# Kernel optimization log

Hardware: AMD Instinct MI355X
Metric: run time of the kernel (lower is better)

The kernel has to match this reference:

```python
import jax, jax.numpy as jnp
import numpy as np

N = 50000      # nodes
E = 800000     # edges (before self-loops)
DIN = 256      # in_channel
H = 1          # heads (PyG GATConv default)
C = 128        # out_channel per head
NEG_SLOPE = 0.2


def setup_inputs() -> dict:
    key = jax.random.key(0)
    k1, k2, k3, k4, k5 = jax.random.split(key, 5)
    x = jax.random.normal(k1, (N, DIN), jnp.float32)
    # random edges guaranteed to have no self-loops (PyG removes then re-adds them)
    src = jax.random.randint(k2, (E,), 0, N, dtype=jnp.int32)
    off = jax.random.randint(k3, (E,), 1, N, dtype=jnp.int32)
    dst = (src + off) % N
    edge_index = jnp.stack([src, dst])  # [2, E], row0=source j, row1=target i
    W = jax.random.normal(k4, (DIN, H * C), jnp.float32) / np.sqrt(DIN)
    att = jax.random.normal(k5, (1, H, 2 * C), jnp.float32) * 0.1
    bias = jnp.zeros((H * C,), jnp.float32)
    return {"x": x, "edge_index": edge_index, "W": W, "att": att, "bias": bias}


def reference(x, edge_index, W, att, bias):
    n = x.shape[0]
    h = (x @ W).reshape(n, H, C)                       # [N,H,C]
    # add self-loops (PyG GATConv forward)
    loops = jnp.arange(n, dtype=edge_index.dtype)
    src = jnp.concatenate([edge_index[0], loops])       # [Et]
    dst = jnp.concatenate([edge_index[1], loops])       # [Et]
    h_i = h[dst]                                        # [Et,H,C] target feats
    h_j = h[src]                                        # [Et,H,C] source feats
    # per-edge attention logit: sum(cat(x_i, x_j) * att)
    alpha = jnp.sum(jnp.concatenate([h_i, h_j], axis=-1) * att, axis=-1)  # [Et,H]
    alpha = jax.nn.leaky_relu(alpha, NEG_SLOPE)
    # segment softmax grouped by destination node (numerically stable)
    amax = jax.ops.segment_max(alpha, dst, num_segments=n)  # [N,H]
    ex = jnp.exp(alpha - amax[dst])
    denom = jax.ops.segment_sum(ex, dst, num_segments=n)    # [N,H]
    a = ex / (denom[dst] + 1e-16)                            # [Et,H]
    # scatter-aggregate weighted source features to targets
    out = jax.ops.segment_sum(h_j * a[..., None], dst, num_segments=n)  # [N,H,C]
    return out.reshape(n, H * C) + bias
```

## Files before the change

kernel.cpp:

```cpp
#include <hip/hip_runtime.h>
#include <hip/hip_bf16.h>

constexpr int N_NODES = 50000;
constexpr int DIN     = 256;
constexpr int C_OUT   = 128;
constexpr int E_EDGES = 800000;
constexpr int ET      = E_EDGES + N_NODES;
constexpr float NEG_SLOPE = 0.2f;

constexpr int NHI      = 196;
constexpr int CAP      = 6144;
constexpr int PEPC     = 8192;
constexpr int NPB_PART = (ET + PEPC - 1) / PEPC;
constexpr int WCONV_BLOCKS = (DIN * C_OUT) / 256;
constexpr int GEMM_RPB    = 64;
constexpr int GEMM_BLOCKS = (N_NODES + GEMM_RPB - 1) / GEMM_RPB;
constexpr int AGG_NPB     = 32;
constexpr int AGG_BLOCKS  = (N_NODES + AGG_NPB - 1) / AGG_NPB;

typedef __attribute__((ext_vector_type(8))) short short8v;
typedef __attribute__((ext_vector_type(4))) float f32x4;

static __device__ __forceinline__ ushort f2bf(float f) {
    __hip_bfloat16 b = __float2bfloat16(f);
    return *reinterpret_cast<ushort*>(&b);
}
static __device__ __forceinline__ short f2bfs(float f) {
    __hip_bfloat16 b = __float2bfloat16(f);
    return *reinterpret_cast<short*>(&b);
}

__global__ __launch_bounds__(256) void part_wconv(const float* __restrict__ W,
                                                  const int* __restrict__ ei,
                                                  ushort* __restrict__ wt,
                                                  int* __restrict__ gcur,
                                                  int* __restrict__ ebuf) {
    const int t = threadIdx.x;
    if (blockIdx.x < NPB_PART) {
        __shared__ int hist[256], basel[256], curl[256];
        const int c = blockIdx.x;
        hist[t] = 0;
        __syncthreads();
        #pragma unroll 4
        for (int i = 0; i < 32; i++) {
            const int e = c * PEPC + i * 256 + t;
            if (e < ET) {
                const int d = (e < E_EDGES) ? ei[E_EDGES + e] : (e - E_EDGES);
                atomicAdd(&hist[d >> 8], 1);
            }
        }
        __syncthreads();
        if (t < NHI) basel[t] = atomicAdd(&gcur[t], hist[t]);
        curl[t] = 0;
        __syncthreads();
        #pragma unroll 4
        for (int i = 0; i < 32; i++) {
            const int e = c * PEPC + i * 256 + t;
            if (e < ET) {
                int s, d;
                if (e < E_EDGES) { s = ei[e]; d = ei[E_EDGES + e]; }
                else             { s = e - E_EDGES; d = s; }
                const int hi = d >> 8;
                const int r = atomicAdd(&curl[hi], 1);
                const int pos = basel[hi] + r;
                if (pos < CAP) ebuf[(size_t)hi * CAP + pos] = ((d & 255) << 16) | s;
            }
        }
        return;
    }
    const int idx = (blockIdx.x - NPB_PART) * 256 + t;
    if (idx < DIN * C_OUT) {
        const int k = idx >> 7, col = idx & 127;
        const int ks = k >> 5, kgrp = (k >> 3) & 3, j = k & 7;
        const int cc = col >> 4, col16 = col & 15;
        wt[((ks * 8 + cc) * 64 + kgrp * 16 + col16) * 8 + j] = f2bf(W[idx]);
    }
}

__global__ __launch_bounds__(256) void gemm_mfma(const float* __restrict__ x,
                                                 const ushort* __restrict__ wt,
                                                 const float* __restrict__ att,
                                                 ushort* __restrict__ hb,
                                                 float* __restrict__ s_dst,
                                                 float* __restrict__ s_src) {
    __shared__ ushort lw[DIN * C_OUT / 2];
    const int t = threadIdx.x;
    const int lane = t & 63, wv = t >> 6;
    const int col16 = lane & 15, kgrp = lane >> 4;
    const int rowbase = blockIdx.x * GEMM_RPB + wv * 16;
    const int hrow = rowbase + col16;
    int r0 = hrow; if (r0 >= N_NODES) r0 = N_NODES - 1;
    const float* xr0 = x + (size_t)r0 * DIN + kgrp * 8;

    f32x4 acc[8] = {};
    const short8v* lwf = (const short8v*)lw;
    #pragma unroll
    for (int ph = 0; ph < 2; ph++) {
        if (ph) __syncthreads();
        {
            const uint4* src = (const uint4*)(wt + ph * (DIN * C_OUT / 2));
            uint4* dst = (uint4*)lw;
            #pragma unroll
            for (int i = 0; i < 8; i++) dst[t + i * 256] = src[t + i * 256];
        }
        short8v A0[4];
        #pragma unroll
        for (int ks = 0; ks < 4; ks++) {
            const int kg = ph * 4 + ks;
            const float4 v0 = *(const float4*)(xr0 + kg * 32);
            const float4 v1 = *(const float4*)(xr0 + kg * 32 + 4);
            short8v a;
            a[0] = f2bfs(v0.x); a[1] = f2bfs(v0.y); a[2] = f2bfs(v0.z); a[3] = f2bfs(v0.w);
            a[4] = f2bfs(v1.x); a[5] = f2bfs(v1.y); a[6] = f2bfs(v1.z); a[7] = f2bfs(v1.w);
            A0[ks] = a;
        }
        __syncthreads();
        #pragma unroll
        for (int ks = 0; ks < 4; ks++) {
            #pragma unroll
            for (int c = 0; c < 8; c++) {
                const short8v bfr = lwf[(ks * 8 + c) * 64 + lane];
                acc[c] = __builtin_amdgcn_mfma_f32_16x16x32_bf16(bfr, A0[ks], acc[c], 0, 0, 0);
            }
        }
    }

    const bool ok = (hrow < N_NODES);
    float pd = 0.f, ps = 0.f;
    #pragma unroll
    for (int c = 0; c < 8; c++) {
        const int colb = c * 16 + kgrp * 4;
        const float4 ad = *(const float4*)(att + colb);
        const float4 as = *(const float4*)(att + C_OUT + colb);
        pd += acc[c][0] * ad.x + acc[c][1] * ad.y + acc[c][2] * ad.z + acc[c][3] * ad.w;
        ps += acc[c][0] * as.x + acc[c][1] * as.y + acc[c][2] * as.z + acc[c][3] * as.w;
        if (ok) {
            uint2 pk;
            pk.x = (uint)(ushort)f2bf(acc[c][0]) | ((uint)(ushort)f2bf(acc[c][1]) << 16);
            pk.y = (uint)(ushort)f2bf(acc[c][2]) | ((uint)(ushort)f2bf(acc[c][3]) << 16);
            *(uint2*)(hb + (size_t)hrow * C_OUT + colb) = pk;
        }
    }
    pd += __shfl_xor(pd, 16); pd += __shfl_xor(pd, 32);
    ps += __shfl_xor(ps, 16); ps += __shfl_xor(ps, 32);
    if (kgrp == 0 && ok) { s_dst[hrow] = pd; s_src[hrow] = ps; }
}

__global__ __launch_bounds__(256) void final_kernel(const int* __restrict__ gcur,
                                                    const int* __restrict__ ebuf,
                                                    int2* __restrict__ offs2,
                                                    int* __restrict__ esrc) {
    __shared__ int histl[256], sA[256], sE[256], curl[256];
    const int t = threadIdx.x, hi = blockIdx.x;
    const int n = min(gcur[hi], CAP);
    const size_t segbase = (size_t)hi * CAP;
    histl[t] = 0;
    __syncthreads();
    for (int k = t; k < n; k += 256)
        atomicAdd(&histl[(ebuf[segbase + k] >> 16) & 255], 1);
    __syncthreads();
    const int v = histl[t];
    sA[t] = v;
    __syncthreads();
    #pragma unroll
    for (int off = 1; off < 256; off <<= 1) {
        const int y = (t >= off) ? sA[t - off] : 0;
        __syncthreads();
        sA[t] += y;
        __syncthreads();
    }
    sE[t] = sA[t] - v;
    curl[t] = 0;
    const int node = hi * 256 + t;
    if (node < N_NODES) {
        const int beg = (int)segbase + sE[t];
        offs2[node] = make_int2(beg, beg + v);
    }
    __syncthreads();
    for (int k = t; k < n; k += 256) {
        const int e2 = ebuf[segbase + k];
        const int lo = (e2 >> 16) & 255;
        const int r = atomicAdd(&curl[lo], 1);
        esrc[segbase + sE[lo] + r] = e2 & 0xFFFF;
    }
}

__global__ __launch_bounds__(256) void aggregate_kernel(
    const ushort* __restrict__ hb, const int2* __restrict__ offs2,
    const int* __restrict__ esrc, const float* __restrict__ s_dst,
    const float* __restrict__ s_src, const float* __restrict__ bias,
    float* __restrict__ out) {
    const int t = threadIdx.x;
    const int wv = t >> 6, lane = t & 63;
    const int sub = lane >> 3, l8 = lane & 7;
    const int node = blockIdx.x * AGG_NPB + wv * 8 + sub;
    const bool valid = (node < N_NODES);

    const int2 be = valid ? offs2[node] : make_int2(0, 0);
    const float sd = valid ? s_dst[node] : 0.f;
    float den = 0.f;
    float acc[16] = {};
    const uint4* __restrict__ h4 = (const uint4*)hb;

    for (int e = be.x; e < be.y; e++) {
        const int s = esrc[e];
        float a = sd + s_src[s];
        a = (a > 0.f) ? a : NEG_SLOPE * a;
        const float w = __expf(a);
        den += w;
        const uint4 hv0 = h4[(size_t)s * 16 + l8];
        const uint4 hv1 = h4[(size_t)s * 16 + 8 + l8];
        acc[0]  += w * __uint_as_float(hv0.x << 16);
        acc[1]  += w * __uint_as_float(hv0.x & 0xffff0000u);
        acc[2]  += w * __uint_as_float(hv0.y << 16);
        acc[3]  += w * __uint_as_float(hv0.y & 0xffff0000u);
        acc[4]  += w * __uint_as_float(hv0.z << 16);
        acc[5]  += w * __uint_as_float(hv0.z & 0xffff0000u);
        acc[6]  += w * __uint_as_float(hv0.w << 16);
        acc[7]  += w * __uint_as_float(hv0.w & 0xffff0000u);
        acc[8]  += w * __uint_as_float(hv1.x << 16);
        acc[9]  += w * __uint_as_float(hv1.x & 0xffff0000u);
        acc[10] += w * __uint_as_float(hv1.y << 16);
        acc[11] += w * __uint_as_float(hv1.y & 0xffff0000u);
        acc[12] += w * __uint_as_float(hv1.z << 16);
        acc[13] += w * __uint_as_float(hv1.z & 0xffff0000u);
        acc[14] += w * __uint_as_float(hv1.w << 16);
        acc[15] += w * __uint_as_float(hv1.w & 0xffff0000u);
    }
    if (!valid) return;
    const float inv = 1.f / (den + 1e-16f);
    float* op = out + (size_t)node * C_OUT;
    #pragma unroll
    for (int half = 0; half < 2; half++) {
        const int base = half * 64 + l8 * 8;
        const float4 b0 = *(const float4*)(bias + base);
        const float4 b1 = *(const float4*)(bias + base + 4);
        float4 o0 = make_float4(acc[half * 8 + 0] * inv + b0.x, acc[half * 8 + 1] * inv + b0.y,
                                acc[half * 8 + 2] * inv + b0.z, acc[half * 8 + 3] * inv + b0.w);
        float4 o1 = make_float4(acc[half * 8 + 4] * inv + b1.x, acc[half * 8 + 5] * inv + b1.y,
                                acc[half * 8 + 6] * inv + b1.z, acc[half * 8 + 7] * inv + b1.w);
        *(float4*)(op + base)     = o0;
        *(float4*)(op + base + 4) = o1;
    }
}

extern "C" void kernel_launch(void* const* d_in, const int* in_sizes, int n_in,
                              void* d_out, int out_size, void* d_ws, size_t ws_size,
                              hipStream_t stream) {
    const float* x    = (const float*)d_in[0];
    const int*   ei   = (const int*)d_in[1];
    const float* W    = (const float*)d_in[2];
    const float* att  = (const float*)d_in[3];
    const float* bias = (const float*)d_in[4];
    float* out = (float*)d_out;

    ushort* wt    = (ushort*)d_ws;
    ushort* hbuf  = wt + DIN * C_OUT;
    int*    ebuf  = (int*)(hbuf + (size_t)N_NODES * C_OUT);
    int*    esrc  = ebuf + (size_t)NHI * CAP;
    float*  s_src = (float*)(esrc + (size_t)NHI * CAP);
    float*  s_dst = s_src + N_NODES;
    int2*   offs2 = (int2*)(s_dst + N_NODES);
    int*    gcur  = (int*)(offs2 + N_NODES);

    hipMemsetAsync(gcur, 0, NHI * sizeof(int), stream);
    part_wconv<<<NPB_PART + WCONV_BLOCKS, 256, 0, stream>>>(W, ei, wt, gcur, ebuf);
    gemm_mfma<<<GEMM_BLOCKS, 256, 0, stream>>>(x, wt, att, hbuf, s_dst, s_src);
    final_kernel<<<NHI, 256, 0, stream>>>(gcur, ebuf, offs2, esrc);
    aggregate_kernel<<<AGG_BLOCKS, 256, 0, stream>>>(
        hbuf, offs2, esrc, s_dst, s_src, bias, out);
}
```

Measured before the change: 101.4 us.

## Fuse CSR finalize into GEMM launch with per-chunk fixed-slot partitioning

Partitioning now writes each chunk's edges into fixed-size per-(bucket,chunk) slots, so one histogram pass, the global atomics and the memset go away. The CSR finalize step runs as extra blocks of the GEMM launch, so one kernel launch is removed and it overlaps with the matmul. Self-loops are no longer stored as edges; the aggregation kernel seeds its accumulators with each node's own term instead. Edges beyond the 96 per bucket-chunk slot cap would be dropped silently. Finalize blocks now scan a sparse, padded segment with per-slot count checks.

```diff
diff --git a/kernel.cpp b/kernel.cpp
--- a/kernel.cpp
+++ b/kernel.cpp
@@ -5,18 +5,19 @@
 constexpr int DIN     = 256;
 constexpr int C_OUT   = 128;
 constexpr int E_EDGES = 800000;
-constexpr int ET      = E_EDGES + N_NODES;
 constexpr float NEG_SLOPE = 0.2f;
 
-constexpr int NHI      = 196;
-constexpr int CAP      = 6144;
-constexpr int PEPC     = 8192;
-constexpr int NPB_PART = (ET + PEPC - 1) / PEPC;
+constexpr int NHI  = 196;
+constexpr int NCH  = 98;
+constexpr int EPC  = 8192;
+constexpr int CPC  = 96;
+constexpr int SEG  = NCH * CPC;
+constexpr int CAPB = 6144;
 constexpr int WCONV_BLOCKS = (DIN * C_OUT) / 256;
-constexpr int GEMM_RPB    = 64;
-constexpr int GEMM_BLOCKS = (N_NODES + GEMM_RPB - 1) / GEMM_RPB;
-constexpr int AGG_NPB     = 32;
-constexpr int AGG_BLOCKS  = (N_NODES + AGG_NPB - 1) / AGG_NPB;
+constexpr int GEMM_RPB     = 64;
+constexpr int GEMM_BLOCKS  = (N_NODES + GEMM_RPB - 1) / GEMM_RPB;
+constexpr int AGG_NPB      = 32;
+constexpr int AGG_BLOCKS   = (N_NODES + AGG_NPB - 1) / AGG_NPB;
 
 typedef __attribute__((ext_vector_type(8))) short short8v;
 typedef __attribute__((ext_vector_type(4))) float f32x4;
@@ -33,42 +34,31 @@
 __global__ __launch_bounds__(256) void part_wconv(const float* __restrict__ W,
                                                   const int* __restrict__ ei,
                                                   ushort* __restrict__ wt,
-                                                  int* __restrict__ gcur,
+                                                  int* __restrict__ cnt2,
                                                   int* __restrict__ ebuf) {
     const int t = threadIdx.x;
-    if (blockIdx.x < NPB_PART) {
-        __shared__ int hist[256], basel[256], curl[256];
+    if (blockIdx.x < NCH) {
+        __shared__ int curl[256];
         const int c = blockIdx.x;
-        hist[t] = 0;
+        curl[t] = 0;
         __syncthreads();
         #pragma unroll 4
         for (int i = 0; i < 32; i++) {
-            const int e = c * PEPC + i * 256 + t;
-            if (e < ET) {
-                const int d = (e < E_EDGES) ? ei[E_EDGES + e] : (e - E_EDGES);
-                atomicAdd(&hist[d >> 8], 1);
-            }
-        }
-        __syncthreads();
-        if (t < NHI) basel[t] = atomicAdd(&gcur[t], hist[t]);
-        curl[t] = 0;
-        __syncthreads();
-        #pragma unroll 4
-        for (int i = 0; i < 32; i++) {
-            const int e = c * PEPC + i * 256 + t;
-            if (e < ET) {
-                int s, d;
-                if (e < E_EDGES) { s = ei[e]; d = ei[E_EDGES + e]; }
-                else             { s = e - E_EDGES; d = s; }
+            const int e = c * EPC + i * 256 + t;
+            if (e < E_EDGES) {
+                const int s = ei[e];
+                const int d = ei[E_EDGES + e];
                 const int hi = d >> 8;
                 const int r = atomicAdd(&curl[hi], 1);
-                const int pos = basel[hi] + r;
-                if (pos < CAP) ebuf[(size_t)hi * CAP + pos] = ((d & 255) << 16) | s;
+                if (r < CPC)
+                    ebuf[(size_t)(hi * NCH + c) * CPC + r] = ((d & 255) << 16) | s;
             }
         }
+        __syncthreads();
+        if (t < NHI) cnt2[t * NCH + c] = min(curl[t], CPC);
         return;
     }
-    const int idx = (blockIdx.x - NPB_PART) * 256 + t;
+    const int idx = (blockIdx.x - NCH) * 256 + t;
     if (idx < DIN * C_OUT) {
         const int k = idx >> 7, col = idx & 127;
         const int ks = k >> 5, kgrp = (k >> 3) & 3, j = k & 7;
@@ -77,17 +67,79 @@
     }
 }
 
-__global__ __launch_bounds__(256) void gemm_mfma(const float* __restrict__ x,
-                                                 const ushort* __restrict__ wt,
-                                                 const float* __restrict__ att,
-                                                 ushort* __restrict__ hb,
-                                                 float* __restrict__ s_dst,
-                                                 float* __restrict__ s_src) {
+__global__ __launch_bounds__(256) void gemm_final(const float* __restrict__ x,
+                                                  const ushort* __restrict__ wt,
+                                                  const float* __restrict__ att,
+                                                  const int* __restrict__ cnt2,
+                                                  const int* __restrict__ ebuf,
+                                                  ushort* __restrict__ hb,
+                                                  float* __restrict__ s_dst,
+                                                  float* __restrict__ s_src,
+                                                  int2* __restrict__ offs2,
+                                                  int* __restrict__ esrc) {
     __shared__ ushort lw[DIN * C_OUT / 2];
     const int t = threadIdx.x;
+
+    if (blockIdx.x >= GEMM_BLOCKS) {
+        int* li    = (int*)lw;
+        int* histl = li;
+        int* sA    = li + 256;
+        int* sE    = li + 512;
+        int* curl  = li + 768;
+        int* cl    = li + 1024;
+        const int hi = blockIdx.x - GEMM_BLOCKS;
+        const int base = hi * SEG;
+        histl[t] = 0;
+        if (t < NCH) cl[t] = cnt2[hi * NCH + t];
+        __syncthreads();
+        #pragma unroll 4
+        for (int i = 0; i < (SEG + 255) / 256; i++) {
+            const int k = i * 256 + t;
+            if (k < SEG) {
+                const int c = k / CPC, r = k - c * CPC;
+                if (r < cl[c])
+                    atomicAdd(&histl[(ebuf[base + k] >> 16) & 255], 1);
+            }
+        }
+        __syncthreads();
+        const int v = histl[t];
+        sA[t] = v;
+        __syncthreads();
+        #pragma unroll
+        for (int off = 1; off < 256; off <<= 1) {
+            const int y = (t >= off) ? sA[t - off] : 0;
+            __syncthreads();
+            sA[t] += y;
+            __syncthreads();
+        }
+        sE[t] = sA[t] - v;
+        curl[t] = 0;
+        const int node = hi * 256 + t;
+        if (node < N_NODES) {
+            const int beg = hi * CAPB + sE[t];
+            offs2[node] = make_int2(beg, beg + v);
+        }
+        __syncthreads();
+        #pragma unroll 4
+        for (int i = 0; i < (SEG + 255) / 256; i++) {
+            const int k = i * 256 + t;
+            if (k < SEG) {
+                const int c = k / CPC, r = k - c * CPC;
+                if (r < cl[c]) {
+                    const int e2 = ebuf[base + k];
+                    const int lo = (e2 >> 16) & 255;
+                    const int rk = atomicAdd(&curl[lo], 1);
+                    esrc[hi * CAPB + sE[lo] + rk] = e2 & 0xFFFF;
+                }
+            }
+        }
+        return;
+    }
+
+    const int gb = blockIdx.x;
     const int lane = t & 63, wv = t >> 6;
     const int col16 = lane & 15, kgrp = lane >> 4;
-    const int rowbase = blockIdx.x * GEMM_RPB + wv * 16;
+    const int rowbase = gb * GEMM_RPB + wv * 16;
     const int hrow = rowbase + col16;
     int r0 = hrow; if (r0 >= N_NODES) r0 = N_NODES - 1;
     const float* xr0 = x + (size_t)r0 * DIN + kgrp * 8;
@@ -146,45 +198,6 @@
     if (kgrp == 0 && ok) { s_dst[hrow] = pd; s_src[hrow] = ps; }
 }
 
-__global__ __launch_bounds__(256) void final_kernel(const int* __restrict__ gcur,
-                                                    const int* __restrict__ ebuf,
-                                                    int2* __restrict__ offs2,
-                                                    int* __restrict__ esrc) {
-    __shared__ int histl[256], sA[256], sE[256], curl[256];
-    const int t = threadIdx.x, hi = blockIdx.x;
-    const int n = min(gcur[hi], CAP);
-    const size_t segbase = (size_t)hi * CAP;
-    histl[t] = 0;
-    __syncthreads();
-    for (int k = t; k < n; k += 256)
-        atomicAdd(&histl[(ebuf[segbase + k] >> 16) & 255], 1);
-    __syncthreads();
-    const int v = histl[t];
-    sA[t] = v;
-    __syncthreads();
-    #pragma unroll
-    for (int off = 1; off < 256; off <<= 1) {
-        const int y = (t >= off) ? sA[t - off] : 0;
-        __syncthreads();
-        sA[t] += y;
-        __syncthreads();
-    }
-    sE[t] = sA[t] - v;
-    curl[t] = 0;
-    const int node = hi * 256 + t;
-    if (node < N_NODES) {
-        const int beg = (int)segbase + sE[t];
-        offs2[node] = make_int2(beg, beg + v);
-    }
-    __syncthreads();
-    for (int k = t; k < n; k += 256) {
-        const int e2 = ebuf[segbase + k];
-        const int lo = (e2 >> 16) & 255;
-        const int r = atomicAdd(&curl[lo], 1);
-        esrc[segbase + sE[lo] + r] = e2 & 0xFFFF;
-    }
-}
-
 __global__ __launch_bounds__(256) void aggregate_kernel(
     const ushort* __restrict__ hb, const int2* __restrict__ offs2,
     const int* __restrict__ esrc, const float* __restrict__ s_dst,
@@ -201,6 +214,31 @@
     float den = 0.f;
     float acc[16] = {};
     const uint4* __restrict__ h4 = (const uint4*)hb;
+
+    if (valid) {
+        float a = sd + s_src[node];
+        a = (a > 0.f) ? a : NEG_SLOPE * a;
+        const float w = __expf(a);
+        den = w;
+        const uint4 hv0 = h4[(size_t)node * 16 + l8];
+        const uint4 hv1 = h4[(size_t)node * 16 + 8 + l8];
+        acc[0]  = w * __uint_as_float(hv0.x << 16);
+        acc[1]  = w * __uint_as_float(hv0.x & 0xffff0000u);
+        acc[2]  = w * __uint_as_float(hv0.y << 16);
+        acc[3]  = w * __uint_as_float(hv0.y & 0xffff0000u);
+        acc[4]  = w * __uint_as_float(hv0.z << 16);
+        acc[5]  = w * __uint_as_float(hv0.z & 0xffff0000u);
+        acc[6]  = w * __uint_as_float(hv0.w << 16);
+        acc[7]  = w * __uint_as_float(hv0.w & 0xffff0000u);
+        acc[8]  = w * __uint_as_float(hv1.x << 16);
+        acc[9]  = w * __uint_as_float(hv1.x & 0xffff0000u);
+        acc[10] = w * __uint_as_float(hv1.y << 16);
+        acc[11] = w * __uint_as_float(hv1.y & 0xffff0000u);
+        acc[12] = w * __uint_as_float(hv1.z << 16);
+        acc[13] = w * __uint_as_float(hv1.z & 0xffff0000u);
+        acc[14] = w * __uint_as_float(hv1.w << 16);
+        acc[15] = w * __uint_as_float(hv1.w & 0xffff0000u);
+    }
 
     for (int e = be.x; e < be.y; e++) {
         const int s = esrc[e];
@@ -257,16 +295,15 @@
     ushort* wt    = (ushort*)d_ws;
     ushort* hbuf  = wt + DIN * C_OUT;
     int*    ebuf  = (int*)(hbuf + (size_t)N_NODES * C_OUT);
-    int*    esrc  = ebuf + (size_t)NHI * CAP;
-    float*  s_src = (float*)(esrc + (size_t)NHI * CAP);
+    int*    esrc  = ebuf + (size_t)NHI * SEG;
+    int*    cnt2  = esrc + (size_t)NHI * CAPB;
+    float*  s_src = (float*)(cnt2 + NHI * NCH);
     float*  s_dst = s_src + N_NODES;
     int2*   offs2 = (int2*)(s_dst + N_NODES);
-    int*    gcur  = (int*)(offs2 + N_NODES);
-
-    hipMemsetAsync(gcur, 0, NHI * sizeof(int), stream);
-    part_wconv<<<NPB_PART + WCONV_BLOCKS, 256, 0, stream>>>(W, ei, wt, gcur, ebuf);
-    gemm_mfma<<<GEMM_BLOCKS, 256, 0, stream>>>(x, wt, att, hbuf, s_dst, s_src);
-    final_kernel<<<NHI, 256, 0, stream>>>(gcur, ebuf, offs2, esrc);
+
+    part_wconv<<<NCH + WCONV_BLOCKS, 256, 0, stream>>>(W, ei, wt, cnt2, ebuf);
+    gemm_final<<<GEMM_BLOCKS + NHI, 256, 0, stream>>>(
+        x, wt, att, cnt2, ebuf, hbuf, s_dst, s_src, offs2, esrc);
     aggregate_kernel<<<AGG_BLOCKS, 256, 0, stream>>>(
         hbuf, offs2, esrc, s_dst, s_src, bias, out);
 }
```

New measurement: 95.95 us. 1.06x faster.
